# Kernel tuning notes

Hardware: AMD Instinct MI355X
Metric: run time of the kernel (lower is better)

## Reference

```python
import jax, jax.numpy as jnp
import numpy as np

N_NODES = 50000
N_GRAPHS = 64


def gcn_layer(x, W, b, src, dst, norm, n):
    # PyG GCNConv: h = x @ W; aggregate norm-weighted messages at dst; add bias
    h = x @ W
    msg = h[src] * norm[:, None]          # [E_tot, out_dim] gather
    out = jax.ops.segment_sum(msg, dst, num_segments=n)
    return out + b


def to_dense_batch(x, batch, max_num, num_graphs):
    n = x.shape[0]
    counts = jax.ops.segment_sum(jnp.ones((n,), x.dtype), batch, num_segments=num_graphs)
    starts = jnp.concatenate([jnp.zeros((1,), jnp.int32),
                              jnp.cumsum(counts.astype(jnp.int32))[:-1]])
    pos = jnp.arange(n, dtype=jnp.int32) - starts[batch]
    valid = pos < max_num
    b_idx = jnp.where(valid, batch, num_graphs)   # overflow -> dummy row
    p_idx = jnp.where(valid, pos, 0)
    dense = jnp.zeros((num_graphs + 1, max_num, x.shape[1]), x.dtype)
    dense = dense.at[b_idx, p_idx].set(x)
    return dense[:num_graphs]


def setup_inputs() -> dict:
    key = jax.random.key(0)
    ks = jax.random.split(key, 12)
    F0, F2, F3, OUT = 54, 108, 216, 200
    x = jax.random.normal(ks[0], (N_NODES, F0), jnp.float32)
    edge_index = jax.random.randint(ks[1], (2, 800000), 0, N_NODES, jnp.int64)
    batch = jnp.sort(jax.random.randint(ks[2], (N_NODES,), 0, N_GRAPHS, jnp.int64))
    def glorot(k, shp):
        lim = 1.0 / np.sqrt(shp[0])
        return jax.random.uniform(k, shp, jnp.float32, -lim, lim)
    return {
        "x": x, "edge_index": edge_index, "batch": batch, "max_num": 1000,
        "W1": glorot(ks[3], (F0, F0)), "b1": jnp.zeros((F0,), jnp.float32),
        "W2": glorot(ks[4], (F0, F2)), "b2": jnp.zeros((F2,), jnp.float32),
        "W3": glorot(ks[5], (F2, F3)), "b3": jnp.zeros((F3,), jnp.float32),
        "Wf": glorot(ks[6], (F3, OUT)), "bf": glorot(ks[7], (OUT,)),
    }


def reference(x, edge_index, batch, max_num, W1, b1, W2, b2, W3, b3, Wf, bf):
    n = x.shape[0]
    loops = jnp.arange(n, dtype=edge_index.dtype)
    src = jnp.concatenate([edge_index[0], loops])
    dst = jnp.concatenate([edge_index[1], loops])
    # symmetric GCN normalization with self-loops (edge_weight = 1)
    deg = jax.ops.segment_sum(jnp.ones_like(dst, jnp.float32), dst, num_segments=n)
    dinv = jax.lax.rsqrt(deg)  # deg >= 1 due to self-loops
    norm = dinv[src] * dinv[dst]

    h = jax.nn.relu(gcn_layer(x, W1, b1, src, dst, norm, n))
    h = jax.nn.relu(gcn_layer(h, W2, b2, src, dst, norm, n))
    h = jax.nn.relu(gcn_layer(h, W3, b3, src, dst, norm, n))
    h = h @ Wf + bf
    return to_dense_batch(h, batch, max_num, N_GRAPHS)
```

## Files before the change

### kernel.cpp

```cpp
#include <hip/hip_runtime.h>
#include <hip/hip_bf16.h>

#define N_GRAPHS 64

typedef __bf16 bf16x8 __attribute__((ext_vector_type(8)));
typedef float floatx4 __attribute__((ext_vector_type(4)));

__device__ __forceinline__ float b2f(unsigned short u) {
    union { unsigned int i; float f; } v;
    v.i = ((unsigned int)u) << 16;
    return v.f;
}
__device__ __forceinline__ unsigned short f2b(float f) {
    __hip_bfloat16 h = __float2bfloat16(f);
    return *(unsigned short*)&h;
}


__global__ void k_deg(const int* __restrict__ dst, int* __restrict__ deg, int E) {
    int e = blockIdx.x * blockDim.x + threadIdx.x;
    if (e < E) atomicAdd(&deg[dst[e]], 1);
}

__global__ void k_scan_blocks(const int* __restrict__ deg, int* __restrict__ row_start,
                              int* __restrict__ blk_sums, int N) {
    __shared__ int s[256];
    int t = threadIdx.x;
    int i = blockIdx.x * 256 + t;
    int v = (i < N) ? deg[i] : 0;
    s[t] = v;
    __syncthreads();
    for (int off = 1; off < 256; off <<= 1) {
        int x = (t >= off) ? s[t - off] : 0;
        __syncthreads();
        s[t] += x;
        __syncthreads();
    }
    if (i < N) row_start[i] = s[t] - v;
    if (t == 255) blk_sums[blockIdx.x] = s[255];
}

__global__ void k_scan_tot(const int* __restrict__ blk_sums, int nb, int* __restrict__ blk_off) {
    __shared__ int s[256];
    int t = threadIdx.x;
    int v = (t < nb) ? blk_sums[t] : 0;
    s[t] = v;
    __syncthreads();
    for (int off = 1; off < 256; off <<= 1) {
        int x = (t >= off) ? s[t - off] : 0;
        __syncthreads();
        s[t] += x;
        __syncthreads();
    }
    if (t < nb) blk_off[t] = s[t] - v;
}

__global__ void k_scan_add(int* __restrict__ row_start, const int* __restrict__ blk_off,
                           int* __restrict__ cursor, const int* __restrict__ deg,
                           float* __restrict__ dinv, const int* __restrict__ batch,
                           int* __restrict__ gstarts, int N, int E) {
    int i = blockIdx.x * 256 + threadIdx.x;
    if (i < N) {
        int r = row_start[i] + blk_off[blockIdx.x];
        row_start[i] = r;
        cursor[i] = r;
        dinv[i] = 1.0f / sqrtf((float)(deg[i] + 1));
        int b = batch[i];
        int prev = (i == 0) ? -1 : batch[i - 1];
        for (int g = prev + 1; g <= b; ++g) gstarts[g] = i;
        if (i == N - 1)
            for (int g = b + 1; g <= N_GRAPHS; ++g) gstarts[g] = N;
    }
    if (i == 0) row_start[N] = E;
}

__global__ void k_fill(const int* __restrict__ src, const int* __restrict__ dst,
                       int* __restrict__ cursor, int2* __restrict__ col2,
                       const float* __restrict__ dinv, int E) {
    int e = blockIdx.x * blockDim.x + threadIdx.x;
    if (e < E) {
        int s = src[e];
        int p = atomicAdd(&cursor[dst[e]], 1);
        col2[p] = make_int2(s, __float_as_int(dinv[s]));
    }
}

__device__ __forceinline__ void swz_one(const float* __restrict__ W,
                                        unsigned short* __restrict__ Wsw, int i, int K, int Nn,
                                        int KS) {
    int j = i & 7, lane = (i >> 3) & 63;
    int ks = (i >> 9) % KS, nt = i / (512 * KS);
    int n = nt * 16 + (lane & 15);
    int k = ks * 32 + (lane >> 4) * 8 + j;
    float v = (k < K && n < Nn) ? W[(size_t)k * Nn + n] : 0.f;
    Wsw[i] = f2b(v);
}

#define T_W1 (4 * 2 * 512)
#define T_W2 (7 * 2 * 512)
#define T_W3 (14 * 4 * 512)
#define T_WF (13 * 7 * 512)

__global__ void k_prep(const float* __restrict__ W1, const float* __restrict__ W2,
                       const float* __restrict__ W3, const float* __restrict__ Wf,
                       unsigned short* __restrict__ W1s, unsigned short* __restrict__ W2s,
                       unsigned short* __restrict__ W3s, unsigned short* __restrict__ Wfs,
                       const float* __restrict__ x, unsigned short* __restrict__ xb, int M) {
    int i = blockIdx.x * 256 + threadIdx.x;
    if (i < T_W1) swz_one(W1, W1s, i, 54, 54, 2);
    else if (i < T_W1 + T_W2) swz_one(W2, W2s, i - T_W1, 54, 108, 2);
    else if (i < T_W1 + T_W2 + T_W3) swz_one(W3, W3s, i - T_W1 - T_W2, 108, 216, 4);
    else if (i < T_W1 + T_W2 + T_W3 + T_WF)
        swz_one(Wf, Wfs, i - T_W1 - T_W2 - T_W3, 216, 200, 7);
    else {
        int ii = i - (T_W1 + T_W2 + T_W3 + T_WF);
        if (ii < M) xb[ii] = f2b(x[ii]);
    }
}


__device__ __forceinline__ void gather54(const unsigned short* __restrict__ in,
                                         const int* __restrict__ row_start,
                                         const int2* __restrict__ col2,
                                         const float* __restrict__ dinv,
                                         unsigned short* agg_s, int node0, int N, int t) {
    constexpr int F = 54, AS = 72;
    int g = t >> 5, s = t & 31;
    for (int r = g; r < 32; r += 8) {
        int n = node0 + r;
        float a0 = 0.f, a1 = 0.f;
        if (n < N && s < 27) {
            float dn = dinv[n];
            ushort2 u = *((const ushort2*)(in + (size_t)n * F) + s);
            a0 = dn * b2f(u.x);
            a1 = dn * b2f(u.y);
            int rs = row_start[n], re = row_start[n + 1];
            int e = rs;
            for (; e + 3 < re; e += 4) {
                int2 c0 = col2[e], c1 = col2[e + 1], c2 = col2[e + 2], c3 = col2[e + 3];
                ushort2 v0 = *((const ushort2*)(in + (size_t)c0.x * F) + s);
                ushort2 v1 = *((const ushort2*)(in + (size_t)c1.x * F) + s);
                ushort2 v2 = *((const ushort2*)(in + (size_t)c2.x * F) + s);
                ushort2 v3 = *((const ushort2*)(in + (size_t)c3.x * F) + s);
                float d0 = __int_as_float(c0.y), d1 = __int_as_float(c1.y);
                float d2 = __int_as_float(c2.y), d3 = __int_as_float(c3.y);
                a0 += d0 * b2f(v0.x) + d1 * b2f(v1.x) + d2 * b2f(v2.x) + d3 * b2f(v3.x);
                a1 += d0 * b2f(v0.y) + d1 * b2f(v1.y) + d2 * b2f(v2.y) + d3 * b2f(v3.y);
            }
            for (; e < re; ++e) {
                int2 c = col2[e];
                ushort2 v = *((const ushort2*)(in + (size_t)c.x * F) + s);
                float d = __int_as_float(c.y);
                a0 += d * b2f(v.x);
                a1 += d * b2f(v.y);
            }
            a0 *= dn;
            a1 *= dn;
        }
        *((ushort2*)(agg_s + r * AS) + s) = make_ushort2(f2b(a0), f2b(a1));
    }
}

__device__ __forceinline__ void gather108(const unsigned short* __restrict__ in,
                                          const int* __restrict__ row_start,
                                          const int2* __restrict__ col2,
                                          const float* __restrict__ dinv,
                                          unsigned short* agg_s, int node0, int N, int t) {
    constexpr int F = 108, AS = 136;
    int g = t >> 5, s = t & 31;
    for (int r = g; r < 32; r += 8) {
        int n = node0 + r;
        float a0 = 0.f, a1 = 0.f, a2 = 0.f, a3 = 0.f;
        if (n < N && s < 27) {
            float dn = dinv[n];
            ushort4 u = *((const ushort4*)(in + (size_t)n * F) + s);
            a0 = dn * b2f(u.x);
            a1 = dn * b2f(u.y);
            a2 = dn * b2f(u.z);
            a3 = dn * b2f(u.w);
            int rs = row_start[n], re = row_start[n + 1];
            int e = rs;
            for (; e + 3 < re; e += 4) {
                int2 c0 = col2[e], c1 = col2[e + 1], c2 = col2[e + 2], c3 = col2[e + 3];
                ushort4 v0 = *((const ushort4*)(in + (size_t)c0.x * F) + s);
                ushort4 v1 = *((const ushort4*)(in + (size_t)c1.x * F) + s);
                ushort4 v2 = *((const ushort4*)(in + (size_t)c2.x * F) + s);
                ushort4 v3 = *((const ushort4*)(in + (size_t)c3.x * F) + s);
                float d0 = __int_as_float(c0.y), d1 = __int_as_float(c1.y);
                float d2 = __int_as_float(c2.y), d3 = __int_as_float(c3.y);
                a0 += d0 * b2f(v0.x) + d1 * b2f(v1.x) + d2 * b2f(v2.x) + d3 * b2f(v3.x);
                a1 += d0 * b2f(v0.y) + d1 * b2f(v1.y) + d2 * b2f(v2.y) + d3 * b2f(v3.y);
                a2 += d0 * b2f(v0.z) + d1 * b2f(v1.z) + d2 * b2f(v2.z) + d3 * b2f(v3.z);
                a3 += d0 * b2f(v0.w) + d1 * b2f(v1.w) + d2 * b2f(v2.w) + d3 * b2f(v3.w);
            }
            for (; e < re; ++e) {
                int2 c = col2[e];
                ushort4 v = *((const ushort4*)(in + (size_t)c.x * F) + s);
                float d = __int_as_float(c.y);
                a0 += d * b2f(v.x);
                a1 += d * b2f(v.y);
                a2 += d * b2f(v.z);
                a3 += d * b2f(v.w);
            }
            a0 *= dn;
            a1 *= dn;
            a2 *= dn;
            a3 *= dn;
        }
        *((ushort4*)(agg_s + r * AS) + s) =
            make_ushort4(f2b(a0), f2b(a1), f2b(a2), f2b(a3));
    }
}


template <int FIN, int FOUT, int KS, int NT, int V>
__global__ __launch_bounds__(256) void k_layer(
    const unsigned short* __restrict__ in, const int* __restrict__ row_start,
    const int2* __restrict__ col2, const float* __restrict__ dinv,
    const unsigned short* __restrict__ Wsw, const float* __restrict__ bias,
    unsigned short* __restrict__ hout, int N) {
    constexpr int AS = KS * 32 + 8;
    __shared__ __align__(16) unsigned short agg_s[32 * AS];
    int node0 = blockIdx.x * 32;
    int t = threadIdx.x;
    if (V == 2)
        gather54(in, row_start, col2, dinv, agg_s, node0, N, t);
    else
        gather108(in, row_start, col2, dinv, agg_s, node0, N, t);
    __syncthreads();
    int lane = t & 63, wv = t >> 6, m = lane & 15, q = lane >> 4;
    bf16x8 a[2][KS];
#pragma unroll
    for (int mt = 0; mt < 2; ++mt)
#pragma unroll
        for (int ks = 0; ks < KS; ++ks)
            a[mt][ks] = *(const bf16x8*)(agg_s + (mt * 16 + m) * AS + ks * 32 + q * 8);
    for (int nt = wv; nt < NT; nt += 4) {
        const unsigned short* bp = Wsw + ((size_t)(nt * KS) * 64 + lane) * 8;
        bf16x8 bfr[KS];
#pragma unroll
        for (int ks = 0; ks < KS; ++ks) bfr[ks] = *(const bf16x8*)(bp + ks * 512);
        int fo = nt * 16 + m;
        float bb = (fo < FOUT) ? bias[fo] : 0.f;
#pragma unroll
        for (int mt = 0; mt < 2; ++mt) {
            floatx4 c = {0.f, 0.f, 0.f, 0.f};
#pragma unroll
            for (int ks = 0; ks < KS; ++ks)
                c = __builtin_amdgcn_mfma_f32_16x16x32_bf16(a[mt][ks], bfr[ks], c, 0, 0, 0);
#pragma unroll
            for (int r = 0; r < 4; ++r) {
                int n = node0 + mt * 16 + q * 4 + r;
                if (n < N && fo < FOUT)
                    hout[(size_t)n * FOUT + fo] = f2b(fmaxf(c[r] + bb, 0.f));
            }
        }
    }
}


__global__ __launch_bounds__(256) void k_l3f(
    const unsigned short* __restrict__ h2, const int* __restrict__ row_start,
    const int2* __restrict__ col2, const float* __restrict__ dinv,
    const unsigned short* __restrict__ W3s, const float* __restrict__ b3,
    const unsigned short* __restrict__ Wfs, const float* __restrict__ bfv,
    const int* __restrict__ batch, const int* __restrict__ gstarts, float* __restrict__ out,
    int N, int mn) {
    constexpr int AS = 136, HS = 232;
    __shared__ __align__(16) unsigned short agg_s[32 * AS];
    __shared__ __align__(16) unsigned short h3_s[32 * HS];
    int node0 = blockIdx.x * 32;
    int t = threadIdx.x;
    gather108(h2, row_start, col2, dinv, agg_s, node0, N, t);
    __syncthreads();
    int lane = t & 63, wv = t >> 6, m = lane & 15, q = lane >> 4;
    bf16x8 a1[2][4];
#pragma unroll
    for (int mt = 0; mt < 2; ++mt)
#pragma unroll
        for (int ks = 0; ks < 4; ++ks)
            a1[mt][ks] = *(const bf16x8*)(agg_s + (mt * 16 + m) * AS + ks * 32 + q * 8);
    for (int nt = wv; nt < 14; nt += 4) {
        const unsigned short* bp = W3s + ((size_t)(nt * 4) * 64 + lane) * 8;
        bf16x8 bf0 = *(const bf16x8*)(bp);
        bf16x8 bf1 = *(const bf16x8*)(bp + 512);
        bf16x8 bf2 = *(const bf16x8*)(bp + 1024);
        bf16x8 bf3 = *(const bf16x8*)(bp + 1536);
        int fo = nt * 16 + m;
        float bb = (fo < 216) ? b3[fo] : 0.f;
#pragma unroll
        for (int mt = 0; mt < 2; ++mt) {
            floatx4 c = {0.f, 0.f, 0.f, 0.f};
            c = __builtin_amdgcn_mfma_f32_16x16x32_bf16(a1[mt][0], bf0, c, 0, 0, 0);
            c = __builtin_amdgcn_mfma_f32_16x16x32_bf16(a1[mt][1], bf1, c, 0, 0, 0);
            c = __builtin_amdgcn_mfma_f32_16x16x32_bf16(a1[mt][2], bf2, c, 0, 0, 0);
            c = __builtin_amdgcn_mfma_f32_16x16x32_bf16(a1[mt][3], bf3, c, 0, 0, 0);
#pragma unroll
            for (int r = 0; r < 4; ++r) {
                int row = mt * 16 + q * 4 + r;
                h3_s[row * HS + fo] = f2b(fmaxf(c[r] + bb, 0.f));
            }
        }
    }
    __syncthreads();
    bf16x8 a2[2][7];
#pragma unroll
    for (int mt = 0; mt < 2; ++mt)
#pragma unroll
        for (int ks = 0; ks < 7; ++ks)
            a2[mt][ks] = *(const bf16x8*)(h3_s + (mt * 16 + m) * HS + ks * 32 + q * 8);
    for (int nt = wv; nt < 13; nt += 4) {
        const unsigned short* bp = Wfs + ((size_t)(nt * 7) * 64 + lane) * 8;
        bf16x8 bfr[7];
#pragma unroll
        for (int ks = 0; ks < 7; ++ks) bfr[ks] = *(const bf16x8*)(bp + ks * 512);
        int fo = nt * 16 + m;
        if (fo >= 200) continue;
        float bb = bfv[fo];
#pragma unroll
        for (int mt = 0; mt < 2; ++mt) {
            floatx4 c = {0.f, 0.f, 0.f, 0.f};
#pragma unroll
            for (int ks = 0; ks < 7; ++ks)
                c = __builtin_amdgcn_mfma_f32_16x16x32_bf16(a2[mt][ks], bfr[ks], c, 0, 0, 0);
#pragma unroll
            for (int r = 0; r < 4; ++r) {
                int n = node0 + mt * 16 + q * 4 + r;
                if (n < N) {
                    int b = batch[n];
                    int pos = n - gstarts[b];
                    if (pos >= 0 && pos < mn)
                        out[((size_t)b * mn + pos) * 200 + fo] = c[r] + bb;
                }
            }
        }
    }
}

extern "C" void kernel_launch(void* const* d_in, const int* in_sizes, int n_in,
                              void* d_out, int out_size, void* d_ws, size_t ws_size,
                              hipStream_t stream) {
    const float* x = (const float*)d_in[0];
    const int* ei = (const int*)d_in[1];
    const int* batch = (const int*)d_in[2];
    const float* W1 = (const float*)d_in[4];
    const float* b1 = (const float*)d_in[5];
    const float* W2 = (const float*)d_in[6];
    const float* b2 = (const float*)d_in[7];
    const float* W3 = (const float*)d_in[8];
    const float* b3 = (const float*)d_in[9];
    const float* Wf = (const float*)d_in[10];
    const float* bfv = (const float*)d_in[11];
    float* out = (float*)d_out;

    const int N = in_sizes[2];
    const int E = in_sizes[1] / 2;
    const int mn = out_size / (N_GRAPHS * 200);
    const int* src = ei;
    const int* dst = ei + E;

    char* w = (char*)d_ws;
    auto alloc = [&](size_t bytes) {
        void* p = (void*)w;
        w += (bytes + 255) & ~(size_t)255;
        return p;
    };
    int* deg = (int*)alloc((size_t)N * 4);
    int* row_start = (int*)alloc((size_t)(N + 1) * 4);
    int* blk_sums = (int*)alloc(256 * 4);
    int* blk_off = (int*)alloc(256 * 4);
    int* cursor = (int*)alloc((size_t)N * 4);
    int2* col2 = (int2*)alloc((size_t)E * 8);
    float* dinv = (float*)alloc((size_t)N * 4);
    int* gstarts = (int*)alloc((N_GRAPHS + 1) * 4);
    unsigned short* xb = (unsigned short*)alloc((size_t)N * 54 * 2);
    unsigned short* h1 = (unsigned short*)alloc((size_t)N * 54 * 2);
    unsigned short* h2 = (unsigned short*)alloc((size_t)N * 108 * 2);
    unsigned short* W1s = (unsigned short*)alloc((size_t)T_W1 * 2);
    unsigned short* W2s = (unsigned short*)alloc((size_t)T_W2 * 2);
    unsigned short* W3s = (unsigned short*)alloc((size_t)T_W3 * 2);
    unsigned short* Wfs = (unsigned short*)alloc((size_t)T_WF * 2);
    (void)ws_size;

    hipMemsetAsync(deg, 0, (size_t)N * 4, stream);
    hipMemsetAsync(d_out, 0, (size_t)out_size * sizeof(float), stream);

    int NB = (N + 255) / 256;
    k_deg<<<(E + 255) / 256, 256, 0, stream>>>(dst, deg, E);
    k_scan_blocks<<<NB, 256, 0, stream>>>(deg, row_start, blk_sums, N);
    k_scan_tot<<<1, 256, 0, stream>>>(blk_sums, NB, blk_off);
    k_scan_add<<<NB, 256, 0, stream>>>(row_start, blk_off, cursor, deg, dinv, batch, gstarts,
                                       N, E);
    k_fill<<<(E + 255) / 256, 256, 0, stream>>>(src, dst, cursor, col2, dinv, E);
    int Mx = N * 54;
    int prep_total = T_W1 + T_W2 + T_W3 + T_WF + Mx;
    k_prep<<<(prep_total + 255) / 256, 256, 0, stream>>>(W1, W2, W3, Wf, W1s, W2s, W3s, Wfs,
                                                         x, xb, Mx);

    int NBL = (N + 31) / 32;
    k_layer<54, 54, 2, 4, 2><<<NBL, 256, 0, stream>>>(xb, row_start, col2, dinv, W1s, b1,
                                                      h1, N);
    k_layer<54, 108, 2, 7, 2><<<NBL, 256, 0, stream>>>(h1, row_start, col2, dinv, W2s, b2,
                                                       h2, N);
    k_l3f<<<NBL, 256, 0, stream>>>(h2, row_start, col2, dinv, W3s, b3, Wfs, bfv, batch,
                                   gstarts, out, N, mn);
}
```

Before: 331.5 us.

## Pad feature rows to 64/128 and gather with 16-byte loads across edge-parallel lanes

Node feature buffers are padded from 54/108 to 64/128 bf16 columns so every row is 16-byte aligned. The gather now has each lane load 8 features with one vector load, and splits a node's edges across several lane groups, combining the partial sums with xor shuffles. The intent is fewer, wider, better-coalesced memory transactions and more parallelism per node in the gather. In exchange it moves more bytes for the padded columns, adds shuffle reductions, and makes layer 2 compute an extra output tile.

Result: faster. 315.0 us (-5.0%).

```diff
diff --git a/kernel.cpp b/kernel.cpp
--- a/kernel.cpp
+++ b/kernel.cpp
@@ -5,6 +5,7 @@
 
 typedef __bf16 bf16x8 __attribute__((ext_vector_type(8)));
 typedef float floatx4 __attribute__((ext_vector_type(4)));
+typedef unsigned short ushort8v __attribute__((ext_vector_type(8)));
 
 __device__ __forceinline__ float b2f(unsigned short u) {
     union { unsigned int i; float f; } v;
@@ -97,7 +98,7 @@
 }
 
 #define T_W1 (4 * 2 * 512)
-#define T_W2 (7 * 2 * 512)
+#define T_W2 (8 * 2 * 512)
 #define T_W3 (14 * 4 * 512)
 #define T_WF (13 * 7 * 512)
 
@@ -105,7 +106,7 @@
                        const float* __restrict__ W3, const float* __restrict__ Wf,
                        unsigned short* __restrict__ W1s, unsigned short* __restrict__ W2s,
                        unsigned short* __restrict__ W3s, unsigned short* __restrict__ Wfs,
-                       const float* __restrict__ x, unsigned short* __restrict__ xb, int M) {
+                       const float* __restrict__ x, unsigned short* __restrict__ xb, int Nn) {
     int i = blockIdx.x * 256 + threadIdx.x;
     if (i < T_W1) swz_one(W1, W1s, i, 54, 54, 2);
     else if (i < T_W1 + T_W2) swz_one(W2, W2s, i - T_W1, 54, 108, 2);
@@ -114,106 +115,69 @@
         swz_one(Wf, Wfs, i - T_W1 - T_W2 - T_W3, 216, 200, 7);
     else {
         int ii = i - (T_W1 + T_W2 + T_W3 + T_WF);
-        if (ii < M) xb[ii] = f2b(x[ii]);
-    }
-}
-
-
-__device__ __forceinline__ void gather54(const unsigned short* __restrict__ in,
-                                         const int* __restrict__ row_start,
-                                         const int2* __restrict__ col2,
-                                         const float* __restrict__ dinv,
-                                         unsigned short* agg_s, int node0, int N, int t) {
-    constexpr int F = 54, AS = 72;
-    int g = t >> 5, s = t & 31;
-    for (int r = g; r < 32; r += 8) {
+        if (ii < Nn * 64) {
+            int n = ii >> 6, c = ii & 63;
+            xb[ii] = (c < 54) ? f2b(x[(size_t)n * 54 + c]) : (unsigned short)0;
+        }
+    }
+}
+
+
+template <int P, int AS>
+__device__ __forceinline__ void gatherP(const unsigned short* __restrict__ in,
+                                        const int* __restrict__ row_start,
+                                        const int2* __restrict__ col2,
+                                        const float* __restrict__ dinv,
+                                        unsigned short* agg_s, int node0, int N, int t) {
+    constexpr int S = P / 8;
+    constexpr int G = 32 / S;
+    int grp = t >> 5, lane5 = t & 31;
+    int j = lane5 / S, cl = lane5 % S;
+    for (int r = grp; r < 32; r += 8) {
         int n = node0 + r;
-        float a0 = 0.f, a1 = 0.f;
-        if (n < N && s < 27) {
+        float a[8] = {0.f, 0.f, 0.f, 0.f, 0.f, 0.f, 0.f, 0.f};
+        if (n < N) {
             float dn = dinv[n];
-            ushort2 u = *((const ushort2*)(in + (size_t)n * F) + s);
-            a0 = dn * b2f(u.x);
-            a1 = dn * b2f(u.y);
+            if (j == 0) {
+                ushort8v u = *((const ushort8v*)(in + (size_t)n * P) + cl);
+#pragma unroll
+                for (int i = 0; i < 8; ++i) a[i] = dn * b2f(u[i]);
+            }
             int rs = row_start[n], re = row_start[n + 1];
-            int e = rs;
-            for (; e + 3 < re; e += 4) {
-                int2 c0 = col2[e], c1 = col2[e + 1], c2 = col2[e + 2], c3 = col2[e + 3];
-                ushort2 v0 = *((const ushort2*)(in + (size_t)c0.x * F) + s);
-                ushort2 v1 = *((const ushort2*)(in + (size_t)c1.x * F) + s);
-                ushort2 v2 = *((const ushort2*)(in + (size_t)c2.x * F) + s);
-                ushort2 v3 = *((const ushort2*)(in + (size_t)c3.x * F) + s);
+            int e = rs + j;
+            for (; e + G < re; e += 2 * G) {
+                int2 c0 = col2[e], c1 = col2[e + G];
+                ushort8v v0 = *((const ushort8v*)(in + (size_t)c0.x * P) + cl);
+                ushort8v v1 = *((const ushort8v*)(in + (size_t)c1.x * P) + cl);
                 float d0 = __int_as_float(c0.y), d1 = __int_as_float(c1.y);
-                float d2 = __int_as_float(c2.y), d3 = __int_as_float(c3.y);
-                a0 += d0 * b2f(v0.x) + d1 * b2f(v1.x) + d2 * b2f(v2.x) + d3 * b2f(v3.x);
-                a1 += d0 * b2f(v0.y) + d1 * b2f(v1.y) + d2 * b2f(v2.y) + d3 * b2f(v3.y);
-            }
-            for (; e < re; ++e) {
+#pragma unroll
+                for (int i = 0; i < 8; ++i) a[i] += d0 * b2f(v0[i]) + d1 * b2f(v1[i]);
+            }
+            if (e < re) {
                 int2 c = col2[e];
-                ushort2 v = *((const ushort2*)(in + (size_t)c.x * F) + s);
+                ushort8v v = *((const ushort8v*)(in + (size_t)c.x * P) + cl);
                 float d = __int_as_float(c.y);
-                a0 += d * b2f(v.x);
-                a1 += d * b2f(v.y);
-            }
-            a0 *= dn;
-            a1 *= dn;
-        }
-        *((ushort2*)(agg_s + r * AS) + s) = make_ushort2(f2b(a0), f2b(a1));
-    }
-}
-
-__device__ __forceinline__ void gather108(const unsigned short* __restrict__ in,
-                                          const int* __restrict__ row_start,
-                                          const int2* __restrict__ col2,
-                                          const float* __restrict__ dinv,
-                                          unsigned short* agg_s, int node0, int N, int t) {
-    constexpr int F = 108, AS = 136;
-    int g = t >> 5, s = t & 31;
-    for (int r = g; r < 32; r += 8) {
-        int n = node0 + r;
-        float a0 = 0.f, a1 = 0.f, a2 = 0.f, a3 = 0.f;
-        if (n < N && s < 27) {
-            float dn = dinv[n];
-            ushort4 u = *((const ushort4*)(in + (size_t)n * F) + s);
-            a0 = dn * b2f(u.x);
-            a1 = dn * b2f(u.y);
-            a2 = dn * b2f(u.z);
-            a3 = dn * b2f(u.w);
-            int rs = row_start[n], re = row_start[n + 1];
-            int e = rs;
-            for (; e + 3 < re; e += 4) {
-                int2 c0 = col2[e], c1 = col2[e + 1], c2 = col2[e + 2], c3 = col2[e + 3];
-                ushort4 v0 = *((const ushort4*)(in + (size_t)c0.x * F) + s);
-                ushort4 v1 = *((const ushort4*)(in + (size_t)c1.x * F) + s);
-                ushort4 v2 = *((const ushort4*)(in + (size_t)c2.x * F) + s);
-                ushort4 v3 = *((const ushort4*)(in + (size_t)c3.x * F) + s);
-                float d0 = __int_as_float(c0.y), d1 = __int_as_float(c1.y);
-                float d2 = __int_as_float(c2.y), d3 = __int_as_float(c3.y);
-                a0 += d0 * b2f(v0.x) + d1 * b2f(v1.x) + d2 * b2f(v2.x) + d3 * b2f(v3.x);
-                a1 += d0 * b2f(v0.y) + d1 * b2f(v1.y) + d2 * b2f(v2.y) + d3 * b2f(v3.y);
-                a2 += d0 * b2f(v0.z) + d1 * b2f(v1.z) + d2 * b2f(v2.z) + d3 * b2f(v3.z);
-                a3 += d0 * b2f(v0.w) + d1 * b2f(v1.w) + d2 * b2f(v2.w) + d3 * b2f(v3.w);
-            }
-            for (; e < re; ++e) {
-                int2 c = col2[e];
-                ushort4 v = *((const ushort4*)(in + (size_t)c.x * F) + s);
-                float d = __int_as_float(c.y);
-                a0 += d * b2f(v.x);
-                a1 += d * b2f(v.y);
-                a2 += d * b2f(v.z);
-                a3 += d * b2f(v.w);
-            }
-            a0 *= dn;
-            a1 *= dn;
-            a2 *= dn;
-            a3 *= dn;
-        }
-        *((ushort4*)(agg_s + r * AS) + s) =
-            make_ushort4(f2b(a0), f2b(a1), f2b(a2), f2b(a3));
-    }
-}
-
-
-template <int FIN, int FOUT, int KS, int NT, int V>
+#pragma unroll
+                for (int i = 0; i < 8; ++i) a[i] += d * b2f(v[i]);
+            }
+#pragma unroll
+            for (int i = 0; i < 8; ++i) a[i] *= dn;
+        }
+#pragma unroll
+        for (int mask = S; mask < 32; mask <<= 1)
+#pragma unroll
+            for (int i = 0; i < 8; ++i) a[i] += __shfl_xor(a[i], mask, 32);
+        if (j == 0) {
+            ushort8v rv;
+#pragma unroll
+            for (int i = 0; i < 8; ++i) rv[i] = f2b(a[i]);
+            *((ushort8v*)(agg_s + r * AS) + cl) = rv;
+        }
+    }
+}
+
+
+template <int P, int FOUT, int FP, int KS, int NT>
 __global__ __launch_bounds__(256) void k_layer(
     const unsigned short* __restrict__ in, const int* __restrict__ row_start,
     const int2* __restrict__ col2, const float* __restrict__ dinv,
@@ -223,10 +187,7 @@
     __shared__ __align__(16) unsigned short agg_s[32 * AS];
     int node0 = blockIdx.x * 32;
     int t = threadIdx.x;
-    if (V == 2)
-        gather54(in, row_start, col2, dinv, agg_s, node0, N, t);
-    else
-        gather108(in, row_start, col2, dinv, agg_s, node0, N, t);
+    gatherP<P, AS>(in, row_start, col2, dinv, agg_s, node0, N, t);
     __syncthreads();
     int lane = t & 63, wv = t >> 6, m = lane & 15, q = lane >> 4;
     bf16x8 a[2][KS];
@@ -251,8 +212,7 @@
 #pragma unroll
             for (int r = 0; r < 4; ++r) {
                 int n = node0 + mt * 16 + q * 4 + r;
-                if (n < N && fo < FOUT)
-                    hout[(size_t)n * FOUT + fo] = f2b(fmaxf(c[r] + bb, 0.f));
+                if (n < N) hout[(size_t)n * FP + fo] = f2b(fmaxf(c[r] + bb, 0.f));
             }
         }
     }
@@ -271,7 +231,7 @@
     __shared__ __align__(16) unsigned short h3_s[32 * HS];
     int node0 = blockIdx.x * 32;
     int t = threadIdx.x;
-    gather108(h2, row_start, col2, dinv, agg_s, node0, N, t);
+    gatherP<128, AS>(h2, row_start, col2, dinv, agg_s, node0, N, t);
     __syncthreads();
     int lane = t & 63, wv = t >> 6, m = lane & 15, q = lane >> 4;
     bf16x8 a1[2][4];
@@ -373,9 +333,9 @@
     int2* col2 = (int2*)alloc((size_t)E * 8);
     float* dinv = (float*)alloc((size_t)N * 4);
     int* gstarts = (int*)alloc((N_GRAPHS + 1) * 4);
-    unsigned short* xb = (unsigned short*)alloc((size_t)N * 54 * 2);
-    unsigned short* h1 = (unsigned short*)alloc((size_t)N * 54 * 2);
-    unsigned short* h2 = (unsigned short*)alloc((size_t)N * 108 * 2);
+    unsigned short* xb = (unsigned short*)alloc((size_t)N * 64 * 2);
+    unsigned short* h1 = (unsigned short*)alloc((size_t)N * 64 * 2);
+    unsigned short* h2 = (unsigned short*)alloc((size_t)N * 128 * 2);
     unsigned short* W1s = (unsigned short*)alloc((size_t)T_W1 * 2);
     unsigned short* W2s = (unsigned short*)alloc((size_t)T_W2 * 2);
     unsigned short* W3s = (unsigned short*)alloc((size_t)T_W3 * 2);
@@ -392,16 +352,15 @@
     k_scan_add<<<NB, 256, 0, stream>>>(row_start, blk_off, cursor, deg, dinv, batch, gstarts,
                                        N, E);
     k_fill<<<(E + 255) / 256, 256, 0, stream>>>(src, dst, cursor, col2, dinv, E);
-    int Mx = N * 54;
-    int prep_total = T_W1 + T_W2 + T_W3 + T_WF + Mx;
+    int prep_total = T_W1 + T_W2 + T_W3 + T_WF + N * 64;
     k_prep<<<(prep_total + 255) / 256, 256, 0, stream>>>(W1, W2, W3, Wf, W1s, W2s, W3s, Wfs,
-                                                         x, xb, Mx);
+                                                         x, xb, N);
 
     int NBL = (N + 31) / 32;
-    k_layer<54, 54, 2, 4, 2><<<NBL, 256, 0, stream>>>(xb, row_start, col2, dinv, W1s, b1,
-                                                      h1, N);
-    k_layer<54, 108, 2, 7, 2><<<NBL, 256, 0, stream>>>(h1, row_start, col2, dinv, W2s, b2,
-                                                       h2, N);
+    k_layer<64, 54, 64, 2, 4><<<NBL, 256, 0, stream>>>(xb, row_start, col2, dinv, W1s, b1,
+                                                       h1, N);
+    k_layer<64, 108, 128, 2, 8><<<NBL, 256, 0, stream>>>(h1, row_start, col2, dinv, W2s, b2,
+                                                         h2, N);
     k_l3f<<<NBL, 256, 0, stream>>>(h2, row_start, col2, dinv, W3s, b3, Wfs, bfv, batch,
                                    gstarts, out, N, mn);
 }
```
